# Kernel tuning notes

Hardware: AMD Instinct MI355X
Metric: run time of the kernel (lower is better)

The kernel has to match this reference:

```python
import jax, jax.numpy as jnp
import numpy as np

B, S, D_MODEL, D_K = 4, 4096, 1024, 128
NEG = jnp.float32(-1e30)  # acts as -inf for masking; exp underflows to exactly 0 in fp32


def setup_inputs() -> dict:
    key = jax.random.key(0)
    ks = jax.random.split(key, 8)
    sc = 1.0 / np.sqrt(D_MODEL)
    x = jax.random.normal(ks[0], (B, S, D_MODEL), jnp.float32)
    padding_mask = (jax.random.uniform(ks[1], (B, S)) > 0.05).astype(jnp.float32)
    Wq = jax.random.normal(ks[2], (D_MODEL, D_K), jnp.float32) * sc
    bq = jax.random.normal(ks[3], (D_K,), jnp.float32) * 0.01
    Wk = jax.random.normal(ks[4], (D_MODEL, D_K), jnp.float32) * sc
    bk = jax.random.normal(ks[5], (D_K,), jnp.float32) * 0.01
    Wv = jax.random.normal(ks[6], (D_MODEL, D_K), jnp.float32) * sc
    bv = jax.random.normal(ks[7], (D_K,), jnp.float32) * 0.01
    return {"x": x, "padding_mask": padding_mask, "Wq": Wq, "bq": bq,
            "Wk": Wk, "bk": bk, "Wv": Wv, "bv": bv}


def reference(x, padding_mask, Wq, bq, Wk, bk, Wv, bv):
    # Self-attention path (enc_dec_layer_input is None), masked=True (causal).
    scale = jnp.sqrt(jnp.float32(Wq.shape[-1]))
    Q = x @ Wq + bq  # [B,S,Dk]
    K = x @ Wk + bk
    V = x @ Wv + bv
    scores = jnp.einsum('bqd,bkd->bqk', Q, K) / scale  # [B,S,S]
    # causal mask (torch: triu(1) filled with -inf) AND padding outer-product mask
    causal = jnp.tril(jnp.ones((S, S), dtype=bool))  # True = allowed
    pm = (padding_mask[:, :, None] * padding_mask[:, None, :]) > 0  # [B,S,S]
    allowed = causal[None] & pm
    scores = jnp.where(allowed, scores, NEG)
    attn = jax.nn.softmax(scores, axis=-1)
    # torch: fully-masked query rows give NaN -> nan_to_num -> 0.
    # A query row is dead iff its own token is padded (diagonal is causally allowed).
    row_alive = padding_mask > 0  # [B,S]
    attn = jnp.where(row_alive[:, :, None], attn, 0.0)
    out = jnp.einsum('bqk,bkd->bqd', attn, V)  # [B,S,Dk]
    return out
```

## Files before the change

### kernel.cpp

```cpp
#include <hip/hip_runtime.h>
#include <hip/hip_bf16.h>
#include <cstdint>

typedef __bf16 bf16x8 __attribute__((ext_vector_type(8)));
typedef float f32x4 __attribute__((ext_vector_type(4)));

#define MFMA16(a, b, c) __builtin_amdgcn_mfma_f32_16x16x32_bf16((a), (b), (c), 0, 0, 0)

__device__ __forceinline__ unsigned short f2bf(float f) {
  union { float f; unsigned u; } v; v.f = f;
  unsigned u = v.u;
  u += 0x7fffu + ((u >> 16) & 1u);
  return (unsigned short)(u >> 16);
}
__device__ __forceinline__ unsigned pk2(float a, float b) {
  __hip_bfloat162 h = __float22bfloat162_rn(make_float2(a, b));
  union { __hip_bfloat162 h; unsigned u; } v; v.h = h; return v.u;
}

__global__ __launch_bounds__(256) void convert_w(
    const float* __restrict__ Wq, const float* __restrict__ Wk,
    const float* __restrict__ Wv, unsigned short* __restrict__ wt) {
  int idx = blockIdx.x * 256 + threadIdx.x;
  int m = idx >> 17;
  int rem = idx & 131071;
  int k = rem >> 7;
  int n = rem & 127;
  const float* W = (m == 0) ? Wq : (m == 1) ? Wk : Wv;
  wt[(size_t)m * 131072 + (size_t)n * 1024 + k] = f2bf(W[(size_t)k * 128 + n]);
}

__global__ __launch_bounds__(256) void qkv_gemm(
    const float* __restrict__ x, const unsigned short* __restrict__ wt_all,
    const float* __restrict__ bq, const float* __restrict__ bk,
    const float* __restrict__ bv,
    unsigned short* __restrict__ Qg, unsigned short* __restrict__ Kg,
    unsigned short* __restrict__ Vtg) {
  __shared__ unsigned short x_lds[128][40];
  __shared__ unsigned short w_lds[128][40];
  const int tid = threadIdx.x;
  const int lane = tid & 63;
  const int w = tid >> 6;
  const int mode = blockIdx.y;
  const int m0 = blockIdx.x * 128;
  const unsigned short* wt = wt_all + (size_t)mode * 131072;
  const float* bias = (mode == 0) ? bq : (mode == 1) ? bk : bv;

  const int wr = (w >> 1) * 64;
  const int wc = (w & 1) * 64;
  const int lr = lane & 15;
  const int lk = (lane >> 4) * 8;

  f32x4 acc[4][4];
#pragma unroll
  for (int m = 0; m < 4; ++m)
#pragma unroll
    for (int n = 0; n < 4; ++n) acc[m][n] = (f32x4){0.f, 0.f, 0.f, 0.f};

  const int srow = tid >> 1;
  const int shalf = (tid & 1) * 16;
  const float* xrow = x + (size_t)(m0 + srow) * 1024 + shalf;
  const unsigned short* wrow = wt + (size_t)srow * 1024 + shalf;

  float4 xa, xb, xc, xd; uint4 wv0, wv1;
  {
    const float4* s4 = (const float4*)xrow;
    xa = s4[0]; xb = s4[1]; xc = s4[2]; xd = s4[3];
    const uint4* ws4 = (const uint4*)wrow;
    wv0 = ws4[0]; wv1 = ws4[1];
  }

  for (int k0 = 0; k0 < 1024; k0 += 32) {
    __syncthreads();
    {
      uint4 w0, w1;
      w0.x = pk2(xa.x, xa.y);  w0.y = pk2(xa.z, xa.w);
      w0.z = pk2(xb.x, xb.y);  w0.w = pk2(xb.z, xb.w);
      w1.x = pk2(xc.x, xc.y);  w1.y = pk2(xc.z, xc.w);
      w1.z = pk2(xd.x, xd.y);  w1.w = pk2(xd.z, xd.w);
      *(uint4*)&x_lds[srow][shalf] = w0;
      *(uint4*)&x_lds[srow][shalf + 8] = w1;
      *(uint4*)&w_lds[srow][shalf] = wv0;
      *(uint4*)&w_lds[srow][shalf + 8] = wv1;
    }
    __syncthreads();
    if (k0 + 32 < 1024) {
      const float4* s4 = (const float4*)(xrow + k0 + 32);
      xa = s4[0]; xb = s4[1]; xc = s4[2]; xd = s4[3];
      const uint4* ws4 = (const uint4*)(wrow + k0 + 32);
      wv0 = ws4[0]; wv1 = ws4[1];
    }
    bf16x8 af[4], bfr[4];
#pragma unroll
    for (int m = 0; m < 4; ++m) af[m] = *(const bf16x8*)&x_lds[wr + m * 16 + lr][lk];
#pragma unroll
    for (int n = 0; n < 4; ++n) bfr[n] = *(const bf16x8*)&w_lds[wc + n * 16 + lr][lk];
#pragma unroll
    for (int m = 0; m < 4; ++m)
#pragma unroll
      for (int n = 0; n < 4; ++n) acc[m][n] = MFMA16(af[m], bfr[n], acc[m][n]);
  }

  float bcol[4];
#pragma unroll
  for (int n = 0; n < 4; ++n) bcol[n] = bias[wc + n * 16 + lr];
#pragma unroll
  for (int m = 0; m < 4; ++m)
#pragma unroll
    for (int n = 0; n < 4; ++n)
#pragma unroll
      for (int r = 0; r < 4; ++r) {
        int grow = m0 + wr + m * 16 + (lane >> 4) * 4 + r;
        int col = wc + n * 16 + lr;
        float val = acc[m][n][r] + bcol[n];
        if (mode == 0) {
          val *= 0.08838834764831845f;
          Qg[(size_t)grow * 128 + col] = f2bf(val);
        } else if (mode == 1) {
          Kg[(size_t)grow * 128 + col] = f2bf(val);
        } else {
          int bb = grow >> 12, s = grow & 4095;
          Vtg[((size_t)bb * 128 + col) * 4096 + s] = f2bf(val);
        }
      }
}

struct AttnLds {
  unsigned short K_lds[64][136];
  unsigned short V_lds[128][72];
  unsigned short P_lds[4][16][72];
};

__device__ __forceinline__ void attn_tiles(
    AttnLds& S, const unsigned short* __restrict__ Kg,
    const unsigned short* __restrict__ Vtg, const float* __restrict__ pmask,
    int b, int q0, int tstart, int tend,
    const bf16x8 (&qf)[4], float (&mrow)[4], float (&lsum)[4], f32x4 (&o)[8]) {
  const int tid = threadIdx.x;
  const int lane = tid & 63;
  const int w = tid >> 6;
  const int lr = lane & 15;
  const int lg = lane >> 4;
  const int lk = lg * 8;

  for (int t = tstart; t < tend; ++t) {
    const int k0 = t * 64;
    __syncthreads();
    {
      int kr = tid >> 2, seg = (tid & 3) * 32;
      const uint4* src = (const uint4*)(Kg + ((size_t)b * 4096 + k0 + kr) * 128 + seg);
      uint4 v0 = src[0], v1 = src[1], v2 = src[2], v3 = src[3];
      uint4* dst = (uint4*)&S.K_lds[kr][seg];
      dst[0] = v0; dst[1] = v1; dst[2] = v2; dst[3] = v3;
      int d = tid >> 1, half = (tid & 1) * 32;
      const uint4* vs = (const uint4*)(Vtg + ((size_t)b * 128 + d) * 4096 + k0 + half);
      uint4 u0 = vs[0], u1 = vs[1], u2 = vs[2], u3 = vs[3];
      uint4* vdst = (uint4*)&S.V_lds[d][half];
      vdst[0] = u0; vdst[1] = u1; vdst[2] = u2; vdst[3] = u3;
    }
    __syncthreads();

    f32x4 sc[4];
#pragma unroll
    for (int f = 0; f < 4; ++f) {
      sc[f] = (f32x4){0.f, 0.f, 0.f, 0.f};
#pragma unroll
      for (int dc = 0; dc < 4; ++dc) {
        bf16x8 kf = *(const bf16x8*)&S.K_lds[f * 16 + lr][dc * 32 + lk];
        sc[f] = MFMA16(qf[dc], kf, sc[f]);
      }
    }
    float pmk[4];
#pragma unroll
    for (int f = 0; f < 4; ++f) pmk[f] = pmask[(size_t)b * 4096 + k0 + f * 16 + lr];

    float alpha[4];
    float p[4][4];
#pragma unroll
    for (int r = 0; r < 4; ++r) {
      const int qrow = q0 + w * 16 + lg * 4 + r;
      float mx = -1e30f;
#pragma unroll
      for (int f = 0; f < 4; ++f) {
        const int kc = k0 + f * 16 + lr;
        float s = (kc <= qrow && pmk[f] > 0.f) ? sc[f][r] : -1e30f;
        p[f][r] = s;
        mx = fmaxf(mx, s);
      }
      mx = fmaxf(mx, __shfl_xor(mx, 1));
      mx = fmaxf(mx, __shfl_xor(mx, 2));
      mx = fmaxf(mx, __shfl_xor(mx, 4));
      mx = fmaxf(mx, __shfl_xor(mx, 8));
      const float mnew = fmaxf(mrow[r], mx);
      alpha[r] = __expf(mrow[r] - mnew);
      mrow[r] = mnew;
      float sum = 0.f;
#pragma unroll
      for (int f = 0; f < 4; ++f) {
        float pv = (p[f][r] < -1e29f) ? 0.f : __expf(p[f][r] - mnew);
        p[f][r] = pv;
        sum += pv;
      }
      sum += __shfl_xor(sum, 1);
      sum += __shfl_xor(sum, 2);
      sum += __shfl_xor(sum, 4);
      sum += __shfl_xor(sum, 8);
      lsum[r] = lsum[r] * alpha[r] + sum;
    }
#pragma unroll
    for (int f = 0; f < 4; ++f)
#pragma unroll
      for (int r = 0; r < 4; ++r) S.P_lds[w][lg * 4 + r][f * 16 + lr] = f2bf(p[f][r]);
#pragma unroll
    for (int n = 0; n < 8; ++n)
#pragma unroll
      for (int r = 0; r < 4; ++r) o[n][r] *= alpha[r];
    __asm__ volatile("s_waitcnt lgkmcnt(0)" ::: "memory");
#pragma unroll
    for (int kc = 0; kc < 2; ++kc) {
      bf16x8 pa = *(const bf16x8*)&S.P_lds[w][lr][kc * 32 + lk];
#pragma unroll
      for (int n = 0; n < 8; ++n) {
        bf16x8 vf = *(const bf16x8*)&S.V_lds[n * 16 + lr][kc * 32 + lk];
        o[n] = MFMA16(pa, vf, o[n]);
      }
    }
  }
}

__global__ __launch_bounds__(256) void attn_fwd(
    const unsigned short* __restrict__ Qg, const unsigned short* __restrict__ Kg,
    const unsigned short* __restrict__ Vtg, const float* __restrict__ pmask,
    float* __restrict__ out) {
  __shared__ AttnLds S;
  const int tid = threadIdx.x;
  const int lane = tid & 63;
  const int w = tid >> 6;
  const int b = blockIdx.y;
  const int q0 = blockIdx.x * 64;
  const int lr = lane & 15;
  const int lg = lane >> 4;
  const int lk = lg * 8;

  bf16x8 qf[4];
  {
    const unsigned short* qp = Qg + ((size_t)b * 4096 + q0 + w * 16 + lr) * 128;
#pragma unroll
    for (int dc = 0; dc < 4; ++dc) qf[dc] = *(const bf16x8*)(qp + dc * 32 + lk);
  }
  float mrow[4], lsum[4];
  f32x4 o[8];
#pragma unroll
  for (int r = 0; r < 4; ++r) { mrow[r] = -1e30f; lsum[r] = 0.f; }
#pragma unroll
  for (int n = 0; n < 8; ++n) o[n] = (f32x4){0.f, 0.f, 0.f, 0.f};

  attn_tiles(S, Kg, Vtg, pmask, b, q0, 0, (q0 >> 6) + 1, qf, mrow, lsum, o);

#pragma unroll
  for (int r = 0; r < 4; ++r) {
    const int qrow = q0 + w * 16 + lg * 4 + r;
    const bool alive = pmask[(size_t)b * 4096 + qrow] > 0.f;
    const float inv = (alive && lsum[r] > 0.f) ? 1.f / lsum[r] : 0.f;
    float* op = out + ((size_t)b * 4096 + qrow) * 128;
#pragma unroll
    for (int n = 0; n < 8; ++n) op[n * 16 + lr] = o[n][r] * inv;
  }
}

__global__ __launch_bounds__(256) void attn_split(
    const unsigned short* __restrict__ Qg, const unsigned short* __restrict__ Kg,
    const unsigned short* __restrict__ Vtg, const float* __restrict__ pmask,
    float* __restrict__ out, float* __restrict__ o_part,
    float* __restrict__ ml_part) {
  __shared__ AttnLds S;
  const int tid = threadIdx.x;
  const int lane = tid & 63;
  const int w = tid >> 6;
  const int L = blockIdx.x;
  const int xcd = L & 7;
  const int b = xcd >> 1;
  const int s = ((L >> 3) << 1) | (xcd & 1);
  int qb, c, nch;
  if (s < 16)      { qb = s;                c = 0;          nch = 1; }
  else if (s < 48) { int t = s - 16; qb = 16 + (t >> 1); c = t & 1;  nch = 2; }
  else if (s < 96) { int t = s - 48; qb = 32 + t / 3;    c = t % 3;  nch = 3; }
  else             { int t = s - 96; qb = 48 + (t >> 2); c = t & 3;  nch = 4; }
  const int q0 = qb * 64;
  const int tstart = c * 16;
  const int tend = min(c * 16 + 16, qb + 1);
  const int lr = lane & 15;
  const int lg = lane >> 4;
  const int lk = lg * 8;

  bf16x8 qf[4];
  {
    const unsigned short* qp = Qg + ((size_t)b * 4096 + q0 + w * 16 + lr) * 128;
#pragma unroll
    for (int dc = 0; dc < 4; ++dc) qf[dc] = *(const bf16x8*)(qp + dc * 32 + lk);
  }
  float mrow[4], lsum[4];
  f32x4 o[8];
#pragma unroll
  for (int r = 0; r < 4; ++r) { mrow[r] = -1e30f; lsum[r] = 0.f; }
#pragma unroll
  for (int n = 0; n < 8; ++n) o[n] = (f32x4){0.f, 0.f, 0.f, 0.f};

  attn_tiles(S, Kg, Vtg, pmask, b, q0, tstart, tend, qf, mrow, lsum, o);

  if (nch == 1) {
#pragma unroll
    for (int r = 0; r < 4; ++r) {
      const int qrow = q0 + w * 16 + lg * 4 + r;
      const bool alive = pmask[(size_t)b * 4096 + qrow] > 0.f;
      const float inv = (alive && lsum[r] > 0.f) ? 1.f / lsum[r] : 0.f;
      float* op = out + ((size_t)b * 4096 + qrow) * 128;
#pragma unroll
      for (int n = 0; n < 8; ++n) op[n * 16 + lr] = o[n][r] * inv;
    }
  } else {
    const int slot = (b * 64 + qb) * 4 + c;
#pragma unroll
    for (int r = 0; r < 4; ++r) {
      const int row = w * 16 + lg * 4 + r;
      float* op = o_part + ((size_t)slot * 64 + row) * 128;
#pragma unroll
      for (int n = 0; n < 8; ++n) op[n * 16 + lr] = o[n][r];
      if (lr == 0) {
        float* mp = ml_part + ((size_t)slot * 64 + row) * 2;
        mp[0] = mrow[r];
        mp[1] = lsum[r];
      }
    }
  }
}

__global__ __launch_bounds__(256) void attn_combine(
    const float* __restrict__ o_part, const float* __restrict__ ml_part,
    const float* __restrict__ pmask, float* __restrict__ out) {
  const int tid = threadIdx.x;
  const int lane = tid & 63;
  const int w = tid >> 6;
  const int g = blockIdx.x * 4 + w;
  const int b = g / 3072;
  const int rem = g % 3072;
  const int qb = 16 + (rem >> 6);
  const int row = rem & 63;
  const int qrow = qb * 64 + row;
  const int nch = (qb >> 4) + 1;
  const int pbase = (b * 64 + qb) * 4;

  float m[4], l[4];
  float M = -1e30f;
  for (int c = 0; c < nch; ++c) {
    const float* mp = ml_part + ((size_t)(pbase + c) * 64 + row) * 2;
    m[c] = mp[0];
    l[c] = mp[1];
    M = fmaxf(M, m[c]);
  }
  float L = 0.f, wgt[4];
  for (int c = 0; c < nch; ++c) {
    wgt[c] = __expf(m[c] - M);
    L += wgt[c] * l[c];
  }
  float2 acc = {0.f, 0.f};
  for (int c = 0; c < nch; ++c) {
    const float2 v = *(const float2*)(o_part + ((size_t)(pbase + c) * 64 + row) * 128 + lane * 2);
    acc.x += wgt[c] * v.x;
    acc.y += wgt[c] * v.y;
  }
  const bool alive = pmask[(size_t)b * 4096 + qrow] > 0.f;
  const float inv = (alive && L > 0.f) ? 1.f / L : 0.f;
  float2* op = (float2*)(out + ((size_t)b * 4096 + qrow) * 128);
  op[lane] = make_float2(acc.x * inv, acc.y * inv);
}

extern "C" void kernel_launch(void* const* d_in, const int* in_sizes, int n_in,
                              void* d_out, int out_size, void* d_ws, size_t ws_size,
                              hipStream_t stream) {
  (void)in_sizes; (void)n_in; (void)out_size;
  const float* x  = (const float*)d_in[0];
  const float* pm = (const float*)d_in[1];
  const float* Wq = (const float*)d_in[2];
  const float* bq = (const float*)d_in[3];
  const float* Wk = (const float*)d_in[4];
  const float* bk = (const float*)d_in[5];
  const float* Wv = (const float*)d_in[6];
  const float* bv = (const float*)d_in[7];
  float* out = (float*)d_out;

  unsigned short* ws  = (unsigned short*)d_ws;
  unsigned short* wt  = ws;
  unsigned short* Qg  = ws + 393216;
  unsigned short* Kg  = Qg + 2097152;
  unsigned short* Vtg = Kg + 2097152;
  float* o_part  = (float*)(ws + 6684672);
  float* ml_part = o_part + 8388608;
  const size_t WS_NEED = 13369344u + (8388608u + 131072u) * 4u;

  convert_w<<<1536, 256, 0, stream>>>(Wq, Wk, Wv, wt);
  qkv_gemm<<<dim3(128, 3), 256, 0, stream>>>(x, wt, bq, bk, bv, Qg, Kg, Vtg);
  if (ws_size >= WS_NEED) {
    attn_split<<<640, 256, 0, stream>>>(Qg, Kg, Vtg, pm, out, o_part, ml_part);
    attn_combine<<<3072, 256, 0, stream>>>(o_part, ml_part, pm, out);
  } else {
    attn_fwd<<<dim3(64, 4), 256, 0, stream>>>(Qg, Kg, Vtg, pm, out);
  }
}
```

Before: 126.7 us.

## Transpose attention MFMAs so each lane owns one query row

Swaps the MFMA operand order so score and output tiles are computed transposed, putting each query row in a single lane's accumulator. Row max and sum reductions now need two cross-lane shuffles per tile instead of four per row, softmax state is a scalar per lane, and P and output are written with packed vector stores. The padding mask is fetched with one ballot per tile, and tiles that lie fully below the diagonal skip the causal comparison. It depends on the new lane-to-element mapping being right and changes the P LDS padding, which may alter bank conflicts.

```diff
diff --git a/kernel.cpp b/kernel.cpp
--- a/kernel.cpp
+++ b/kernel.cpp
@@ -128,20 +128,21 @@
 struct AttnLds {
   unsigned short K_lds[64][136];
   unsigned short V_lds[128][72];
-  unsigned short P_lds[4][16][72];
+  unsigned short P_lds[4][16][68];
 };
 
 __device__ __forceinline__ void attn_tiles(
     AttnLds& S, const unsigned short* __restrict__ Kg,
     const unsigned short* __restrict__ Vtg, const float* __restrict__ pmask,
     int b, int q0, int tstart, int tend,
-    const bf16x8 (&qf)[4], float (&mrow)[4], float (&lsum)[4], f32x4 (&o)[8]) {
+    const bf16x8 (&qf)[4], float& mrow, float& lsum, f32x4 (&o)[8]) {
   const int tid = threadIdx.x;
   const int lane = tid & 63;
   const int w = tid >> 6;
   const int lr = lane & 15;
   const int lg = lane >> 4;
   const int lk = lg * 8;
+  const int q_own = q0 + w * 16 + lr;
 
   for (int t = tstart; t < tend; ++t) {
     const int k0 = t * 64;
@@ -160,61 +161,68 @@
     }
     __syncthreads();
 
-    f32x4 sc[4];
+    f32x4 st[4];
 #pragma unroll
     for (int f = 0; f < 4; ++f) {
-      sc[f] = (f32x4){0.f, 0.f, 0.f, 0.f};
+      st[f] = (f32x4){0.f, 0.f, 0.f, 0.f};
 #pragma unroll
       for (int dc = 0; dc < 4; ++dc) {
         bf16x8 kf = *(const bf16x8*)&S.K_lds[f * 16 + lr][dc * 32 + lk];
-        sc[f] = MFMA16(qf[dc], kf, sc[f]);
+        st[f] = MFMA16(kf, qf[dc], st[f]);
       }
     }
-    float pmk[4];
-#pragma unroll
-    for (int f = 0; f < 4; ++f) pmk[f] = pmask[(size_t)b * 4096 + k0 + f * 16 + lr];
-
-    float alpha[4];
-    float p[4][4];
-#pragma unroll
-    for (int r = 0; r < 4; ++r) {
-      const int qrow = q0 + w * 16 + lg * 4 + r;
-      float mx = -1e30f;
-#pragma unroll
-      for (int f = 0; f < 4; ++f) {
-        const int kc = k0 + f * 16 + lr;
-        float s = (kc <= qrow && pmk[f] > 0.f) ? sc[f][r] : -1e30f;
-        p[f][r] = s;
-        mx = fmaxf(mx, s);
-      }
-      mx = fmaxf(mx, __shfl_xor(mx, 1));
-      mx = fmaxf(mx, __shfl_xor(mx, 2));
-      mx = fmaxf(mx, __shfl_xor(mx, 4));
-      mx = fmaxf(mx, __shfl_xor(mx, 8));
-      const float mnew = fmaxf(mrow[r], mx);
-      alpha[r] = __expf(mrow[r] - mnew);
-      mrow[r] = mnew;
-      float sum = 0.f;
-#pragma unroll
-      for (int f = 0; f < 4; ++f) {
-        float pv = (p[f][r] < -1e29f) ? 0.f : __expf(p[f][r] - mnew);
-        p[f][r] = pv;
-        sum += pv;
-      }
-      sum += __shfl_xor(sum, 1);
-      sum += __shfl_xor(sum, 2);
-      sum += __shfl_xor(sum, 4);
-      sum += __shfl_xor(sum, 8);
-      lsum[r] = lsum[r] * alpha[r] + sum;
-    }
-#pragma unroll
-    for (int f = 0; f < 4; ++f)
-#pragma unroll
-      for (int r = 0; r < 4; ++r) S.P_lds[w][lg * 4 + r][f * 16 + lr] = f2bf(p[f][r]);
-#pragma unroll
-    for (int n = 0; n < 8; ++n)
-#pragma unroll
-      for (int r = 0; r < 4; ++r) o[n][r] *= alpha[r];
+
+    const unsigned long long mb = __ballot(pmask[(size_t)b * 4096 + k0 + lane] > 0.f);
+    unsigned nib[4];
+#pragma unroll
+    for (int f = 0; f < 4; ++f) nib[f] = (unsigned)(mb >> (16 * f + 4 * lg)) & 0xFu;
+
+    float mx = -1e30f;
+    if (k0 + 63 > q0 + (w << 4)) {
+#pragma unroll
+      for (int f = 0; f < 4; ++f)
+#pragma unroll
+        for (int r = 0; r < 4; ++r) {
+          const bool ok = (((nib[f] >> r) & 1u) != 0u) &&
+                          (k0 + 16 * f + 4 * lg + r <= q_own);
+          const float s = ok ? st[f][r] : -1e30f;
+          st[f][r] = s;
+          mx = fmaxf(mx, s);
+        }
+    } else {
+#pragma unroll
+      for (int f = 0; f < 4; ++f)
+#pragma unroll
+        for (int r = 0; r < 4; ++r) {
+          const bool ok = ((nib[f] >> r) & 1u) != 0u;
+          const float s = ok ? st[f][r] : -1e30f;
+          st[f][r] = s;
+          mx = fmaxf(mx, s);
+        }
+    }
+    mx = fmaxf(mx, __shfl_xor(mx, 16));
+    mx = fmaxf(mx, __shfl_xor(mx, 32));
+    const float mnew = fmaxf(mrow, mx);
+    const float alpha = __expf(mrow - mnew);
+    mrow = mnew;
+
+    float sum = 0.f;
+#pragma unroll
+    for (int f = 0; f < 4; ++f) {
+      const float p0 = (st[f][0] < -1e29f) ? 0.f : __expf(st[f][0] - mnew);
+      const float p1 = (st[f][1] < -1e29f) ? 0.f : __expf(st[f][1] - mnew);
+      const float p2 = (st[f][2] < -1e29f) ? 0.f : __expf(st[f][2] - mnew);
+      const float p3 = (st[f][3] < -1e29f) ? 0.f : __expf(st[f][3] - mnew);
+      sum += (p0 + p1) + (p2 + p3);
+      uint2 u; u.x = pk2(p0, p1); u.y = pk2(p2, p3);
+      *(uint2*)&S.P_lds[w][lr][16 * f + 4 * lg] = u;
+    }
+    sum += __shfl_xor(sum, 16);
+    sum += __shfl_xor(sum, 32);
+    lsum = lsum * alpha + sum;
+#pragma unroll
+    for (int n = 0; n < 8; ++n) o[n] *= alpha;
+
     __asm__ volatile("s_waitcnt lgkmcnt(0)" ::: "memory");
 #pragma unroll
     for (int kc = 0; kc < 2; ++kc) {
@@ -222,7 +230,7 @@
 #pragma unroll
       for (int n = 0; n < 8; ++n) {
         bf16x8 vf = *(const bf16x8*)&S.V_lds[n * 16 + lr][kc * 32 + lk];
-        o[n] = MFMA16(pa, vf, o[n]);
+        o[n] = MFMA16(vf, pa, o[n]);
       }
     }
   }
@@ -248,23 +256,21 @@
 #pragma unroll
     for (int dc = 0; dc < 4; ++dc) qf[dc] = *(const bf16x8*)(qp + dc * 32 + lk);
   }
-  float mrow[4], lsum[4];
+  float mrow = -1e30f, lsum = 0.f;
   f32x4 o[8];
 #pragma unroll
-  for (int r = 0; r < 4; ++r) { mrow[r] = -1e30f; lsum[r] = 0.f; }
-#pragma unroll
   for (int n = 0; n < 8; ++n) o[n] = (f32x4){0.f, 0.f, 0.f, 0.f};
 
   attn_tiles(S, Kg, Vtg, pmask, b, q0, 0, (q0 >> 6) + 1, qf, mrow, lsum, o);
 
-#pragma unroll
-  for (int r = 0; r < 4; ++r) {
-    const int qrow = q0 + w * 16 + lg * 4 + r;
-    const bool alive = pmask[(size_t)b * 4096 + qrow] > 0.f;
-    const float inv = (alive && lsum[r] > 0.f) ? 1.f / lsum[r] : 0.f;
-    float* op = out + ((size_t)b * 4096 + qrow) * 128;
-#pragma unroll
-    for (int n = 0; n < 8; ++n) op[n * 16 + lr] = o[n][r] * inv;
+  const int qrow = q0 + w * 16 + lr;
+  const bool alive = pmask[(size_t)b * 4096 + qrow] > 0.f;
+  const float inv = (alive && lsum > 0.f) ? 1.f / lsum : 0.f;
+  float* op = out + ((size_t)b * 4096 + qrow) * 128 + 4 * lg;
+#pragma unroll
+  for (int n = 0; n < 8; ++n) {
+    f32x4 v = o[n] * inv;
+    *(f32x4*)(op + n * 16) = v;
   }
 }
 
@@ -299,38 +305,32 @@
 #pragma unroll
     for (int dc = 0; dc < 4; ++dc) qf[dc] = *(const bf16x8*)(qp + dc * 32 + lk);
   }
-  float mrow[4], lsum[4];
+  float mrow = -1e30f, lsum = 0.f;
   f32x4 o[8];
 #pragma unroll
-  for (int r = 0; r < 4; ++r) { mrow[r] = -1e30f; lsum[r] = 0.f; }
-#pragma unroll
   for (int n = 0; n < 8; ++n) o[n] = (f32x4){0.f, 0.f, 0.f, 0.f};
 
   attn_tiles(S, Kg, Vtg, pmask, b, q0, tstart, tend, qf, mrow, lsum, o);
 
   if (nch == 1) {
-#pragma unroll
-    for (int r = 0; r < 4; ++r) {
-      const int qrow = q0 + w * 16 + lg * 4 + r;
-      const bool alive = pmask[(size_t)b * 4096 + qrow] > 0.f;
-      const float inv = (alive && lsum[r] > 0.f) ? 1.f / lsum[r] : 0.f;
-      float* op = out + ((size_t)b * 4096 + qrow) * 128;
-#pragma unroll
-      for (int n = 0; n < 8; ++n) op[n * 16 + lr] = o[n][r] * inv;
+    const int qrow = q0 + w * 16 + lr;
+    const bool alive = pmask[(size_t)b * 4096 + qrow] > 0.f;
+    const float inv = (alive && lsum > 0.f) ? 1.f / lsum : 0.f;
+    float* op = out + ((size_t)b * 4096 + qrow) * 128 + 4 * lg;
+#pragma unroll
+    for (int n = 0; n < 8; ++n) {
+      f32x4 v = o[n] * inv;
+      *(f32x4*)(op + n * 16) = v;
     }
   } else {
     const int slot = (b * 64 + qb) * 4 + c;
-#pragma unroll
-    for (int r = 0; r < 4; ++r) {
-      const int row = w * 16 + lg * 4 + r;
-      float* op = o_part + ((size_t)slot * 64 + row) * 128;
-#pragma unroll
-      for (int n = 0; n < 8; ++n) op[n * 16 + lr] = o[n][r];
-      if (lr == 0) {
-        float* mp = ml_part + ((size_t)slot * 64 + row) * 2;
-        mp[0] = mrow[r];
-        mp[1] = lsum[r];
-      }
+    float* op = o_part + ((size_t)slot * 64 + w * 16 + lr) * 128 + 4 * lg;
+#pragma unroll
+    for (int n = 0; n < 8; ++n) *(f32x4*)(op + n * 16) = o[n];
+    if (lane < 16) {
+      float* mp = ml_part + ((size_t)slot * 64 + w * 16 + lane) * 2;
+      mp[0] = mrow;
+      mp[1] = lsum;
     }
   }
 }
```

Result: faster. 123.7 us (-2.4%).
